# Kernel tuning notes

Measured on AMD Instinct MI355X. Metric: run time of the kernel, lower is better.

Reference implementation:

```python
import jax, jax.numpy as jnp
import numpy as np

B, N, HID, H, M = 4, 16384, 512, 8, 32
D = HID // H  # 64


def setup_inputs() -> dict:
    key = jax.random.key(0)
    ks = jax.random.split(key, 8)
    s = 0.02
    return {
        "x": jax.random.normal(ks[0], (B, N, HID), jnp.float32),
        "wkv": jax.random.normal(ks[1], (2 * HID, HID), jnp.float32) * s,
        "bkv": jnp.zeros((2 * HID,), jnp.float32),
        "wtq": jax.random.normal(ks[2], (H, M, D), jnp.float32) * s,
        "alpha1": jnp.ones((H,), jnp.float32),
        "mix1_w": jax.random.normal(ks[3], (H * M, H * M), jnp.float32) * (1.0 / np.sqrt(H * M)),
        "ln1_w": jnp.ones((D,), jnp.float32),
        "ln1_b": jnp.zeros((D,), jnp.float32),
        "wqkv": jax.random.normal(ks[4], (3 * HID, HID), jnp.float32) * s,
        "wout": jax.random.normal(ks[5], (HID, HID), jnp.float32) * s,
        "bout": jnp.zeros((HID,), jnp.float32),
    }


def _layernorm(x, w, b, eps=1e-5):
    mu = x.mean(-1, keepdims=True)
    var = ((x - mu) ** 2).mean(-1, keepdims=True)
    return (x - mu) * jax.lax.rsqrt(var + eps) * w + b


def reference(x, wkv, bkv, wtq, alpha1, mix1_w, ln1_w, ln1_b, wqkv, wout, bout):
    # key/value projection: [B, N, 2*HID]
    kv = x @ wkv.T + bkv
    xk, xv = jnp.split(kv, 2, axis=-1)
    xk = xk.reshape(B, N, H, D).transpose(0, 2, 1, 3)  # b h n d
    xv = xv.reshape(B, N, H, D).transpose(0, 2, 1, 3)
    # slice scores + 1x1 conv head-mixing over the (H*M) channel dim
    scores = jnp.einsum('hmd,bhnd->bhmn', wtq, xk)
    scores = jnp.einsum('oc,bcn->bon', mix1_w, scores.reshape(B, H * M, N)).reshape(B, H, M, N)
    # softmax over the slice dim M (dim=-2)
    sw = jax.nn.softmax(scores * alpha1[:, None, None], axis=-2)  # b h m n
    # weighted reduction to slice tokens, normalized by total weight per slice
    tok = jnp.einsum('bhmn,bhnd->bhmd', sw, xv)
    tok = tok / (sw.sum(axis=-1, keepdims=True) + 1e-5)
    tok = _layernorm(tok, ln1_w, ln1_b)
    tok = tok.transpose(0, 2, 1, 3).reshape(B, M, HID)  # b m (h d)
    # small inner MHA over the M=32 slice tokens
    qkv = tok @ wqkv.T
    q, k, v = jnp.split(qkv, 3, axis=-1)
    q = q.reshape(B, M, H, D).transpose(0, 2, 1, 3)
    k = k.reshape(B, M, H, D).transpose(0, 2, 1, 3)
    v = v.reshape(B, M, H, D).transpose(0, 2, 1, 3)
    dots = jnp.einsum('bhqd,bhkd->bhqk', q, k) * (D ** -0.5)
    attn = jax.nn.softmax(dots, axis=-1)
    out_tok = jnp.einsum('bhqk,bhkd->bhqd', attn, v)
    # broadcast slice tokens back to the N points via slice weights
    out = jnp.einsum('bhmd,bhmn->bhnd', out_tok, sw)
    out = out.transpose(0, 2, 1, 3).reshape(B, N, HID)
    out = out @ wout.T + bout
    return (out, sw, alpha1[:, None, None], jnp.zeros((H, M), jnp.float32), attn)
```

## Files before the change

### kernel.cpp

```cpp
#include <hip/hip_runtime.h>
#include <hip/hip_bf16.h>

#define B_ 4
#define N_ 16384
#define HID_ 512
#define H_ 8
#define M_ 32
#define D_ 64
#define HM_ 256

typedef __hip_bfloat16 bf16;
typedef __bf16 bf16x8 __attribute__((ext_vector_type(8)));
typedef float f32x4 __attribute__((ext_vector_type(4)));

__device__ __forceinline__ void gl_lds16(const bf16* g, bf16* l) {
    __builtin_amdgcn_global_load_lds(
        (const __attribute__((address_space(1))) void*)g,
        (__attribute__((address_space(3))) void*)l, 16, 0, 0);
}

__device__ __forceinline__ int xcd_swz(int lin, int nwg) {
    return (lin & 7) * (nwg >> 3) + (lin >> 3);
}

__device__ __forceinline__ void stage_tile_sw(const bf16* __restrict__ G, long long r0,
        int kk, int ld, bf16* lds, int t) {
    const int l = t & 63, w = t >> 6;
    const int srow = l >> 3;
    const int skel = ((l & 7) ^ srow) * 8;
#pragma unroll
    for (int j = 0; j < 4; ++j) {
        int q = j * 4 + w;
        gl_lds16(G + (r0 + q * 8 + srow) * (long long)ld + kk + skel, lds + q * 512);
    }
}

__device__ __forceinline__ void mfma_half_sw(const bf16* As, const bf16* Bs,
        int l, int wm, int wn, f32x4 acc[4][4]) {
    const int l15 = l & 15;
    const int xsw = (l & 7) * 8;
    const int kq = (l >> 4) * 8;
    __builtin_amdgcn_s_setprio(1);
#pragma unroll
    for (int ks = 0; ks < 64; ks += 32) {
        const int ko = (ks + kq) ^ xsw;
        bf16x8 af[4], bfr[4];
#pragma unroll
        for (int mf = 0; mf < 4; ++mf)
            af[mf] = *(const bf16x8*)(As + (wm * 64 + mf * 16 + l15) * 64 + ko);
#pragma unroll
        for (int nf = 0; nf < 4; ++nf)
            bfr[nf] = *(const bf16x8*)(Bs + (wn * 64 + nf * 16 + l15) * 64 + ko);
#pragma unroll
        for (int mf = 0; mf < 4; ++mf)
#pragma unroll
            for (int nf = 0; nf < 4; ++nf)
                acc[mf][nf] = __builtin_amdgcn_mfma_f32_16x16x32_bf16(af[mf], bfr[nf], acc[mf][nf], 0, 0, 0);
    }
    __builtin_amdgcn_s_setprio(0);
}

template<int NT>
__device__ __forceinline__ void gemm_cnt(
        const bf16* __restrict__ Ag, const bf16* __restrict__ Bg,
        long long arow0, int bcol0, int lda, int ldb,
        bf16 (*As)[8192], bf16 (*Bs)[8192], f32x4 acc[4][4]) {
    const int t = threadIdx.x;
    const int l = t & 63, w = t >> 6;
    const int wm = w >> 1, wn = w & 1;
    stage_tile_sw(Ag, arow0, 0, lda, As[0], t);
    stage_tile_sw(Bg, bcol0, 0, ldb, Bs[0], t);
#pragma unroll
    for (int kt = 0; kt < NT; ++kt) {
        const int cur = kt & 1;
        if (kt + 1 < NT) {
            stage_tile_sw(Ag, arow0, (kt + 1) * 64, lda, As[cur ^ 1], t);
            stage_tile_sw(Bg, bcol0, (kt + 1) * 64, ldb, Bs[cur ^ 1], t);
            asm volatile("s_waitcnt vmcnt(8)" ::: "memory");
        } else {
            asm volatile("s_waitcnt vmcnt(0)" ::: "memory");
        }
        __builtin_amdgcn_s_barrier();
        mfma_half_sw(As[cur], Bs[cur], l, wm, wn, acc);
        __builtin_amdgcn_s_barrier();
    }
}

__global__ __launch_bounds__(256) void k_cast4(const float* __restrict__ s,
        ushort* __restrict__ d) {
    long long i = (long long)blockIdx.x * 256 + threadIdx.x;
    float4 v = reinterpret_cast<const float4*>(s)[i];
    ushort4 o;
    bf16 a0 = __float2bfloat16(v.x), a1 = __float2bfloat16(v.y);
    bf16 a2 = __float2bfloat16(v.z), a3 = __float2bfloat16(v.w);
    o.x = *(ushort*)&a0; o.y = *(ushort*)&a1; o.z = *(ushort*)&a2; o.w = *(ushort*)&a3;
    reinterpret_cast<ushort4*>(d)[i] = o;
}

__global__ __launch_bounds__(256) void k_prep(const float* __restrict__ mix1,
        const float* __restrict__ wtq, const float* __restrict__ wkv,
        const float* __restrict__ bkv, const float* __restrict__ alpha1,
        bf16* __restrict__ wv_sc, float* __restrict__ bias768) {
    __shared__ float wfrow[512];
    __shared__ float red[256];
    const int o = blockIdx.x, t = threadIdx.x;
#pragma unroll
    for (int half = 0; half < 2; ++half) {
        int k = half * 256 + t;
        int h = k >> 6, dd = k & 63;
        float s = 0.f;
#pragma unroll
        for (int m = 0; m < 32; ++m)
            s += mix1[(long long)o * 256 + h * 32 + m] * wtq[((long long)h * 32 + m) * 64 + dd];
        wfrow[k] = s;
    }
    __syncthreads();
    const float al = alpha1[o >> 5];
    float a0 = 0.f, a1 = 0.f;
    for (int c = 0; c < 512; ++c) {
        float wv = wfrow[c];
        a0 += wv * wkv[(long long)c * 512 + t];
        a1 += wv * wkv[(long long)c * 512 + t + 256];
    }
    wv_sc[(long long)(512 + o) * 512 + t] = __float2bfloat16(a0 * al);
    wv_sc[(long long)(512 + o) * 512 + t + 256] = __float2bfloat16(a1 * al);
    float p = wfrow[t] * bkv[t] + wfrow[t + 256] * bkv[t + 256];
    red[t] = p; __syncthreads();
    for (int s = 128; s >= 1; s >>= 1) {
        if (t < s) red[t] += red[t + s];
        __syncthreads();
    }
    if (t == 0) bias768[512 + o] = red[0] * al;
    if (t < 2) bias768[o * 2 + t] = bkv[512 + o * 2 + t];
#pragma unroll
    for (int j = 0; j < 4; ++j) {
        int idx = j * 256 + t;
        int r = 2 * o + (idx >> 9), col = idx & 511;
        wv_sc[(long long)r * 512 + col]
            = __float2bfloat16(wkv[(long long)(512 + r) * 512 + col]);
    }
}

__global__ __launch_bounds__(256) void k12_mfma(const bf16* __restrict__ xb,
        const bf16* __restrict__ wv_sc, const float* __restrict__ bias768,
        bf16* __restrict__ xv, float* __restrict__ swout,
        bf16* __restrict__ sw_bt, float* __restrict__ part) {
    __shared__ __align__(16) bf16 As[2][8192];
    __shared__ __align__(16) bf16 Bs[2][8192];
    f32x4 acc[4][4];
#pragma unroll
    for (int i = 0; i < 4; ++i)
#pragma unroll
        for (int j = 0; j < 4; ++j) acc[i][j] = (f32x4)(0.0f);
    const int wg = xcd_swz(blockIdx.y * 6 + blockIdx.x, 3072);
    const int bx = wg % 6, by = wg / 6;
    const long long arow0 = (long long)by * 128;
    const int bcol0 = bx * 128;
    gemm_cnt<8>(xb, wv_sc, arow0, bcol0, 512, 512, As, Bs, acc);

    const int t = threadIdx.x;
    const int l = t & 63, w = t >> 6, wm = w >> 1, wn = w & 1;
    const int l15 = l & 15, lq = l >> 4;
#pragma unroll
    for (int nf = 0; nf < 4; ++nf) {
        float bv = bias768[bcol0 + wn * 64 + nf * 16 + l15];
#pragma unroll
        for (int mf = 0; mf < 4; ++mf)
#pragma unroll
            for (int r = 0; r < 4; ++r) acc[mf][nf][r] += bv;
    }

    if (bcol0 >= 512) {
#pragma unroll
        for (int mf = 0; mf < 4; ++mf)
#pragma unroll
            for (int r = 0; r < 4; ++r)
#pragma unroll
                for (int g = 0; g < 2; ++g) {
                    float v0 = acc[mf][2 * g][r], v1 = acc[mf][2 * g + 1][r];
                    float mx = fmaxf(v0, v1);
#pragma unroll
                    for (int mk = 1; mk <= 8; mk <<= 1) mx = fmaxf(mx, __shfl_xor(mx, mk));
                    float e0 = __expf(v0 - mx), e1 = __expf(v1 - mx);
                    float s = e0 + e1;
#pragma unroll
                    for (int mk = 1; mk <= 8; mk <<= 1) s += __shfl_xor(s, mk);
                    float ri = 1.f / s;
                    acc[mf][2 * g][r] = e0 * ri;
                    acc[mf][2 * g + 1][r] = e1 * ri;
                }
        {
            float* cpart = (float*)&As[0][0];
#pragma unroll
            for (int nf = 0; nf < 4; ++nf) {
                float ps = 0.f;
#pragma unroll
                for (int mf = 0; mf < 4; ++mf)
#pragma unroll
                    for (int r = 0; r < 4; ++r) ps += acc[mf][nf][r];
                ps += __shfl_xor(ps, 16);
                ps += __shfl_xor(ps, 32);
                if (lq == 0) cpart[wm * 128 + wn * 64 + nf * 16 + l15] = ps;
            }
            __syncthreads();
            if (t < 128)
                part[(long long)by * 256 + (bcol0 - 512) + t] = cpart[t] + cpart[128 + t];
        }
        const int b = (int)(arow0 >> 14);
        const int nbase = (int)(arow0 & 16383) + wm * 64;
#pragma unroll
        for (int mf = 0; mf < 4; ++mf) {
            long long rowb = arow0 + wm * 64 + mf * 16 + lq * 4;
#pragma unroll
            for (int nf = 0; nf < 4; ++nf) {
                int cglob = (bcol0 - 512) + wn * 64 + nf * 16 + l15;
                float4 v = {acc[mf][nf][0], acc[mf][nf][1], acc[mf][nf][2], acc[mf][nf][3]};
                *reinterpret_cast<float4*>(swout + ((long long)b * HM_ + cglob) * N_
                                           + nbase + mf * 16 + lq * 4) = v;
#pragma unroll
                for (int r = 0; r < 4; ++r)
                    sw_bt[(rowb + r) * 256 + cglob] = __float2bfloat16(acc[mf][nf][r]);
            }
        }
    } else {
#pragma unroll
        for (int mf = 0; mf < 4; ++mf) {
            long long rowb = arow0 + wm * 64 + mf * 16 + lq * 4;
#pragma unroll
            for (int nf = 0; nf < 4; ++nf) {
                int col = bcol0 + wn * 64 + nf * 16 + l15;
#pragma unroll
                for (int r = 0; r < 4; ++r)
                    xv[(rowb + r) * 512 + col] = __float2bfloat16(acc[mf][nf][r]);
            }
        }
    }
}

__global__ __launch_bounds__(256) void k3_tok(const bf16* __restrict__ sw_bt,
        const bf16* __restrict__ xv, float* __restrict__ tok_part) {
    __shared__ __align__(16) float smem[17408];
    float (*swsT)[36] = reinterpret_cast<float(*)[36]>(smem);
    bf16* xvs = reinterpret_cast<bf16*>(smem + 9216);
    const int t = threadIdx.x;
    const int chunk = blockIdx.x;
    const int bh = blockIdx.y;
    const int b = bh >> 3, h = bh & 7;
    const int l = t & 63, w = t >> 6;
    const int nlh = l >> 5, mtile = (l >> 3) & 3, dtile = l & 7;
    const int m0 = mtile * 8, d0 = dtile * 8;
    float acc[8][8] = {};
    const int wbase = w * 64;

    for (int pass = 0; pass < 2; ++pass) {
        const int n0 = chunk * 512 + pass * 256;
        {
            const long long base = ((long long)(b * N_ + n0 + t)) * 256 + h * 32;
            const uint4* sp = reinterpret_cast<const uint4*>(sw_bt + base);
            uint4 qs[4] = {sp[0], sp[1], sp[2], sp[3]};
            const uint* qu = reinterpret_cast<const uint*>(qs);
#pragma unroll
            for (int j = 0; j < 16; ++j) {
                uint u = qu[j];
                swsT[t][2 * j] = __uint_as_float(u << 16);
                swsT[t][2 * j + 1] = __uint_as_float(u & 0xffff0000u);
            }
        }
        {
            const uint* xg = reinterpret_cast<const uint*>(xv + ((long long)b * N_ + n0) * 512 + h * 64);
            uint* xls = reinterpret_cast<uint*>(xvs);
#pragma unroll
            for (int p = 0; p < 32; ++p) {
                int idx = p * 256 + t;
                int nl = idx >> 5, prt = idx & 31;
                xls[nl * 32 + prt] = xg[(long long)nl * 256 + prt];
            }
        }
        __syncthreads();
        for (int i = 0; i < 32; ++i) {
            int nl = wbase + i * 2 + nlh;
            float4 s0 = *reinterpret_cast<const float4*>(&swsT[nl][m0]);
            float4 s1 = *reinterpret_cast<const float4*>(&swsT[nl][m0 + 4]);
            uint4 xi = *reinterpret_cast<const uint4*>(&xvs[nl * 64 + d0]);
            float xvf[8];
            xvf[0] = __uint_as_float(xi.x << 16); xvf[1] = __uint_as_float(xi.x & 0xffff0000u);
            xvf[2] = __uint_as_float(xi.y << 16); xvf[3] = __uint_as_float(xi.y & 0xffff0000u);
            xvf[4] = __uint_as_float(xi.z << 16); xvf[5] = __uint_as_float(xi.z & 0xffff0000u);
            xvf[6] = __uint_as_float(xi.w << 16); xvf[7] = __uint_as_float(xi.w & 0xffff0000u);
            float sm[8] = {s0.x, s0.y, s0.z, s0.w, s1.x, s1.y, s1.z, s1.w};
#pragma unroll
            for (int mi = 0; mi < 8; ++mi)
#pragma unroll
                for (int di = 0; di < 8; ++di)
                    acc[mi][di] += sm[mi] * xvf[di];
        }
        __syncthreads();
    }

    float* red = smem;
    float* rb = red + (w * 2 + nlh) * 2048;
#pragma unroll
    for (int mi = 0; mi < 8; ++mi) {
        float4 lo = {acc[mi][0], acc[mi][1], acc[mi][2], acc[mi][3]};
        float4 hi = {acc[mi][4], acc[mi][5], acc[mi][6], acc[mi][7]};
        *reinterpret_cast<float4*>(&rb[(m0 + mi) * 64 + d0]) = lo;
        *reinterpret_cast<float4*>(&rb[(m0 + mi) * 64 + d0 + 4]) = hi;
    }
    __syncthreads();
#pragma unroll
    for (int pp = 0; pp < 2; ++pp) {
        int idx4 = pp * 1024 + t * 4;
        float4 s = {0.f, 0.f, 0.f, 0.f};
#pragma unroll
        for (int r = 0; r < 8; ++r) {
            float4 v = *reinterpret_cast<const float4*>(&red[r * 2048 + idx4]);
            s.x += v.x; s.y += v.y; s.z += v.z; s.w += v.w;
        }
        *reinterpret_cast<float4*>(&tok_part[((long long)bh * 32 + chunk) * 2048 + idx4]) = s;
    }
}

__global__ __launch_bounds__(64) void k4a_ln(const float* __restrict__ tok_part,
        const float* __restrict__ part, const float* __restrict__ ln_w,
        const float* __restrict__ ln_b, float* __restrict__ tok_ln) {
    const int bid = blockIdx.x;
    const int bh = bid >> 5, m = bid & 31;
    const int d = threadIdx.x;
    float s = 0.f;
    for (int ch = 0; ch < 32; ++ch)
        s += tok_part[(((long long)bh * 32 + ch) * 32 + m) * 64 + d];
    const int b = bid >> 8, c = bid & 255;
    float ssum = part[((long long)(b * 128 + d)) * 256 + c]
               + part[((long long)(b * 128 + 64 + d)) * 256 + c];
#pragma unroll
    for (int mk = 32; mk >= 1; mk >>= 1) ssum += __shfl_xor(ssum, mk, 64);
    float tokv = s / (ssum + 1e-5f);
    float mu = tokv;
#pragma unroll
    for (int mk = 32; mk >= 1; mk >>= 1) mu += __shfl_xor(mu, mk, 64);
    mu *= (1.f / 64.f);
    float df = tokv - mu;
    float var = df * df;
#pragma unroll
    for (int mk = 32; mk >= 1; mk >>= 1) var += __shfl_xor(var, mk, 64);
    var *= (1.f / 64.f);
    float y = df * rsqrtf(var + 1e-5f) * ln_w[d] + ln_b[d];
    const int bb = bh >> 3, h = bh & 7;
    tok_ln[((long long)bb * 32 + m) * 512 + h * 64 + d] = y;
}

__global__ __launch_bounds__(256) void k_wqT(const float* __restrict__ wq,
        float* __restrict__ wqT) {
    __shared__ float tile[32][33];
    const int k0 = blockIdx.x * 32;
    const int j0 = blockIdx.y * 32;
    const int tx = threadIdx.x & 31, ty = threadIdx.x >> 5;
#pragma unroll
    for (int r = 0; r < 32; r += 8)
        tile[ty + r][tx] = wq[(long long)(j0 + ty + r) * 512 + k0 + tx];
    __syncthreads();
#pragma unroll
    for (int r = 0; r < 32; r += 8)
        wqT[(long long)(k0 + ty + r) * 1536 + j0 + tx] = tile[tx][ty + r];
}

__global__ __launch_bounds__(256) void k4b_qkv(const float* __restrict__ tok_ln,
        const float* __restrict__ wqT, float* __restrict__ qkv) {
    const int j = (blockIdx.x % 6) * 256 + threadIdx.x;
    const int r0 = (blockIdx.x / 6) * 4;
    float a0 = 0, a1 = 0, a2 = 0, a3 = 0;
    for (int k = 0; k < 512; ++k) {
        float wv = wqT[(long long)k * 1536 + j];
        a0 += tok_ln[(r0 + 0) * 512 + k] * wv;
        a1 += tok_ln[(r0 + 1) * 512 + k] * wv;
        a2 += tok_ln[(r0 + 2) * 512 + k] * wv;
        a3 += tok_ln[(r0 + 3) * 512 + k] * wv;
    }
    qkv[(long long)(r0 + 0) * 1536 + j] = a0;
    qkv[(long long)(r0 + 1) * 1536 + j] = a1;
    qkv[(long long)(r0 + 2) * 1536 + j] = a2;
    qkv[(long long)(r0 + 3) * 1536 + j] = a3;
}

__global__ __launch_bounds__(256) void k4c_attn(const float* __restrict__ qkv,
        float* __restrict__ out_tok, float* __restrict__ attn_out) {
    __shared__ float qsT[64][33], ksT[64][33], vsT[64][33];
    __shared__ float att[32][33];
    __shared__ float rinv[32];
    const int t = threadIdx.x;
    const int bid = blockIdx.x;
    const int b = bid >> 3, h = bid & 7;
#pragma unroll
    for (int i = 0; i < 8; ++i) {
        int idx = i * 256 + t;
        int mi = idx >> 6, dd = idx & 63;
        long long base = ((long long)b * 32 + mi) * 1536 + h * 64 + dd;
        qsT[dd][mi] = qkv[base];
        ksT[dd][mi] = qkv[base + 512];
        vsT[dd][mi] = qkv[base + 1024];
    }
    __syncthreads();
#pragma unroll
    for (int i = 0; i < 4; ++i) {
        int idx = i * 256 + t;
        int qi = idx >> 5, ki = idx & 31;
        float s = 0.f;
#pragma unroll
        for (int dd = 0; dd < 64; ++dd) s += qsT[dd][qi] * ksT[dd][ki];
        att[qi][ki] = s * 0.125f;
    }
    __syncthreads();
    if (t < 32) {
        float mx = -1e30f;
        for (int k = 0; k < 32; ++k) mx = fmaxf(mx, att[t][k]);
        float sum = 0.f;
        for (int k = 0; k < 32; ++k) { float e = __expf(att[t][k] - mx); att[t][k] = e; sum += e; }
        rinv[t] = 1.f / sum;
    }
    __syncthreads();
#pragma unroll
    for (int i = 0; i < 4; ++i) {
        int idx = i * 256 + t;
        int qi = idx >> 5, ki = idx & 31;
        float a = att[qi][ki] * rinv[qi];
        att[qi][ki] = a;
        attn_out[(long long)bid * 1024 + qi * 32 + ki] = a;
    }
    __syncthreads();
#pragma unroll
    for (int i = 0; i < 8; ++i) {
        int idx = i * 256 + t;
        int qi = idx >> 6, dd = idx & 63;
        float s = 0.f;
#pragma unroll
        for (int ki = 0; ki < 32; ++ki) s += att[qi][ki] * vsT[dd][ki];
        out_tok[((long long)bid * 32 + qi) * 64 + dd] = s;
    }
}

__global__ __launch_bounds__(256) void k5_w2(const float* __restrict__ wout,
        const float* __restrict__ out_tok, bf16* __restrict__ W2) {
    const int bid = blockIdx.x;
    const int b = bid >> 9, o = bid & 511;
    const int t = threadIdx.x;
    const int h = t >> 5, m = t & 31;
    float s = 0.f;
#pragma unroll
    for (int dd = 0; dd < 64; ++dd)
        s += wout[(long long)o * 512 + h * 64 + dd]
           * out_tok[(((long long)b * 8 + h) * 32 + m) * 64 + dd];
    W2[(long long)bid * 256 + t] = __float2bfloat16(s);
}

__global__ __launch_bounds__(256) void k6_mfma(const bf16* __restrict__ sw_bt,
        const bf16* __restrict__ W2, const float* __restrict__ bout,
        float* __restrict__ out) {
    __shared__ __align__(16) bf16 As[2][8192];
    __shared__ __align__(16) bf16 Bs[2][8192];
    f32x4 acc[4][4];
#pragma unroll
    for (int i = 0; i < 4; ++i)
#pragma unroll
        for (int j = 0; j < 4; ++j) acc[i][j] = (f32x4)(0.0f);
    const int wg = xcd_swz((blockIdx.z * 128 + blockIdx.y) * 4 + blockIdx.x, 2048);
    const int bx = wg & 3, by = (wg >> 2) & 127, bz = wg >> 9;
    const long long arow0 = (long long)by * 128;
    const int bcol0 = bx * 128;
    gemm_cnt<4>(sw_bt + (long long)bz * N_ * 256, W2 + (long long)bz * 512 * 256,
                arow0, bcol0, 256, 256, As, Bs, acc);
    const int l = threadIdx.x & 63, w = threadIdx.x >> 6;
    const int wm = w >> 1, wn = w & 1;
#pragma unroll
    for (int mf = 0; mf < 4; ++mf) {
#pragma unroll
        for (int nf = 0; nf < 4; ++nf) {
            int col = bcol0 + wn * 64 + nf * 16 + (l & 15);
            float bv = bout[col];
#pragma unroll
            for (int r = 0; r < 4; ++r) {
                long long row = arow0 + wm * 64 + mf * 16 + (l >> 4) * 4 + r;
                out[((long long)bz * N_ + row) * 512 + col] = acc[mf][nf][r] + bv;
            }
        }
    }
}

__global__ void k_misc(const float* __restrict__ alpha1,
        float* __restrict__ outA, float* __restrict__ outZ) {
    int t = threadIdx.x;
    if (t < 8) outA[t] = alpha1[t];
    outZ[t] = 0.f;
}

extern "C" void kernel_launch(void* const* d_in, const int* in_sizes, int n_in,
                              void* d_out, int out_size, void* d_ws, size_t ws_size,
                              hipStream_t stream) {
    const float* x      = (const float*)d_in[0];
    const float* wkv    = (const float*)d_in[1];
    const float* bkv    = (const float*)d_in[2];
    const float* wtq    = (const float*)d_in[3];
    const float* alpha1 = (const float*)d_in[4];
    const float* mix1_w = (const float*)d_in[5];
    const float* ln1_w  = (const float*)d_in[6];
    const float* ln1_b  = (const float*)d_in[7];
    const float* wqkv   = (const float*)d_in[8];
    const float* wout   = (const float*)d_in[9];
    const float* bout   = (const float*)d_in[10];

    float* out    = (float*)d_out;
    float* swout  = out + 33554432LL;
    float* alphaO = out + 50331648LL;
    float* zerosO = out + 50331656LL;
    float* attnO  = out + 50331912LL;

    char* ws = (char*)d_ws;
    bf16*  xb        = (bf16*)(ws);
    float* wqkvT     = (float*)(ws);
    float* part      = (float*)(ws + 67108864LL);
    bf16*  sw_bt     = (bf16*)(ws + 100663296LL);
    bf16*  xv        = (bf16*)(ws + 134217728LL);
    float* tok_part  = (float*)(ws + 201326592LL);
    float* tok_ln    = (float*)(ws + 218107904LL);
    float* qkv       = (float*)(ws + 218370048LL);
    float* out_tok   = (float*)(ws + 219156480LL);
    bf16*  W2b       = (bf16*)(ws + 219418624LL);
    bf16*  wv_sc     = (bf16*)(ws + 220467200LL);
    float* bias768   = (float*)(ws + 221253632LL);

    k_prep<<<256, 256, 0, stream>>>(mix1_w, wtq, wkv, bkv, alpha1, wv_sc, bias768);
    k_cast4<<<32768, 256, 0, stream>>>(x, (ushort*)xb);
    k12_mfma<<<dim3(6, 512), 256, 0, stream>>>(xb, wv_sc, bias768, xv, swout, sw_bt, part);
    k_wqT<<<dim3(16, 48), 256, 0, stream>>>(wqkv, wqkvT);
    k3_tok<<<dim3(32, 32), 256, 0, stream>>>(sw_bt, xv, tok_part);
    k4a_ln<<<1024, 64, 0, stream>>>(tok_part, part, ln1_w, ln1_b, tok_ln);
    k4b_qkv<<<192, 256, 0, stream>>>(tok_ln, wqkvT, qkv);
    k4c_attn<<<32, 256, 0, stream>>>(qkv, out_tok, attnO);
    k5_w2<<<2048, 256, 0, stream>>>(wout, out_tok, W2b);
    k6_mfma<<<dim3(4, 128, 4), 256, 0, stream>>>(sw_bt, W2b, bout, out);
    k_misc<<<1, 256, 0, stream>>>(alpha1, alphaO, zerosO);
}
```

Before: 328.5 us.

## Fuse fp32-to-bf16 cast of x into the projection GEMM A-tile load

```diff
diff --git a/kernel.cpp b/kernel.cpp
--- a/kernel.cpp
+++ b/kernel.cpp
@@ -17,6 +17,16 @@
     __builtin_amdgcn_global_load_lds(
         (const __attribute__((address_space(1))) void*)g,
         (__attribute__((address_space(3))) void*)l, 16, 0, 0);
+}
+__device__ __forceinline__ void gl_lds16f(const float* g, float* l) {
+    __builtin_amdgcn_global_load_lds(
+        (const __attribute__((address_space(1))) void*)g,
+        (__attribute__((address_space(3))) void*)l, 16, 0, 0);
+}
+
+__device__ __forceinline__ uint bpk(float lo, float hi) {
+    bf16 a = __float2bfloat16(lo), b = __float2bfloat16(hi);
+    return (uint)(*(ushort*)&a) | ((uint)(*(ushort*)&b) << 16);
 }
 
 __device__ __forceinline__ int xcd_swz(int lin, int nwg) {
@@ -86,15 +96,81 @@
     }
 }
 
-__global__ __launch_bounds__(256) void k_cast4(const float* __restrict__ s,
-        ushort* __restrict__ d) {
-    long long i = (long long)blockIdx.x * 256 + threadIdx.x;
-    float4 v = reinterpret_cast<const float4*>(s)[i];
-    ushort4 o;
-    bf16 a0 = __float2bfloat16(v.x), a1 = __float2bfloat16(v.y);
-    bf16 a2 = __float2bfloat16(v.z), a3 = __float2bfloat16(v.w);
-    o.x = *(ushort*)&a0; o.y = *(ushort*)&a1; o.z = *(ushort*)&a2; o.w = *(ushort*)&a3;
-    reinterpret_cast<ushort4*>(d)[i] = o;
+__device__ __forceinline__ void stage_a32(const float* __restrict__ G, long long r0,
+        int kk, int ld, float* lds, int t) {
+    const int l = t & 63, w = t >> 6;
+    const int srow = l >> 3;
+    const int sblk = (l & 7) >> 1, half = l & 1;
+    const int scol = ((sblk ^ (srow & 3)) * 8) + half * 4;
+#pragma unroll
+    for (int j = 0; j < 4; ++j) {
+        int q = j * 4 + w;
+        gl_lds16f(G + (r0 + q * 8 + srow) * (long long)ld + kk + scol, lds + q * 256);
+    }
+}
+__device__ __forceinline__ void stage_b32(const bf16* __restrict__ G, long long r0,
+        int kk, int ld, bf16* lds, int t) {
+    const int l = t & 63, w = t >> 6;
+    const int srow = l >> 2;
+    const int scol = ((l & 3) ^ (srow & 3)) * 8;
+#pragma unroll
+    for (int j = 0; j < 2; ++j) {
+        int q = j * 4 + w;
+        gl_lds16(G + (r0 + q * 16 + srow) * (long long)ld + kk + scol, lds + q * 512);
+    }
+}
+
+__device__ __forceinline__ void mfma_step32(const float* Af, const bf16* Bs,
+        int l, int wm, int wn, f32x4 acc[4][4]) {
+    const int l15 = l & 15;
+    const int kb = l >> 4;
+    const int sw8 = (kb ^ (l15 & 3)) * 8;
+    __builtin_amdgcn_s_setprio(1);
+    bf16x8 af[4], bfr[4];
+#pragma unroll
+    for (int mf = 0; mf < 4; ++mf) {
+        const float* ap = Af + (wm * 64 + mf * 16 + l15) * 32 + sw8;
+        float4 v0 = *(const float4*)ap, v1 = *(const float4*)(ap + 4);
+        union { uint4 u; bf16x8 h; } c;
+        c.u.x = bpk(v0.x, v0.y); c.u.y = bpk(v0.z, v0.w);
+        c.u.z = bpk(v1.x, v1.y); c.u.w = bpk(v1.z, v1.w);
+        af[mf] = c.h;
+    }
+#pragma unroll
+    for (int nf = 0; nf < 4; ++nf)
+        bfr[nf] = *(const bf16x8*)(Bs + (wn * 64 + nf * 16 + l15) * 32 + sw8);
+#pragma unroll
+    for (int mf = 0; mf < 4; ++mf)
+#pragma unroll
+        for (int nf = 0; nf < 4; ++nf)
+            acc[mf][nf] = __builtin_amdgcn_mfma_f32_16x16x32_bf16(af[mf], bfr[nf], acc[mf][nf], 0, 0, 0);
+    __builtin_amdgcn_s_setprio(0);
+}
+
+template<int NT>
+__device__ __forceinline__ void gemm_f32a(
+        const float* __restrict__ Ag, const bf16* __restrict__ Bg,
+        long long arow0, int bcol0, int lda, int ldb,
+        float (*Af)[4096], bf16 (*Bs)[4096], f32x4 acc[4][4]) {
+    const int t = threadIdx.x;
+    const int l = t & 63, w = t >> 6;
+    const int wm = w >> 1, wn = w & 1;
+    stage_a32(Ag, arow0, 0, lda, Af[0], t);
+    stage_b32(Bg, bcol0, 0, ldb, Bs[0], t);
+#pragma unroll
+    for (int kt = 0; kt < NT; ++kt) {
+        const int cur = kt & 1;
+        if (kt + 1 < NT) {
+            stage_a32(Ag, arow0, (kt + 1) * 32, lda, Af[cur ^ 1], t);
+            stage_b32(Bg, bcol0, (kt + 1) * 32, ldb, Bs[cur ^ 1], t);
+            asm volatile("s_waitcnt vmcnt(6)" ::: "memory");
+        } else {
+            asm volatile("s_waitcnt vmcnt(0)" ::: "memory");
+        }
+        __builtin_amdgcn_s_barrier();
+        mfma_step32(Af[cur], Bs[cur], l, wm, wn, acc);
+        __builtin_amdgcn_s_barrier();
+    }
 }
 
 __global__ __launch_bounds__(256) void k_prep(const float* __restrict__ mix1,
@@ -141,12 +217,12 @@
     }
 }
 
-__global__ __launch_bounds__(256) void k12_mfma(const bf16* __restrict__ xb,
+__global__ __launch_bounds__(256) void k12_mfma(const float* __restrict__ x,
         const bf16* __restrict__ wv_sc, const float* __restrict__ bias768,
         bf16* __restrict__ xv, float* __restrict__ swout,
         bf16* __restrict__ sw_bt, float* __restrict__ part) {
-    __shared__ __align__(16) bf16 As[2][8192];
-    __shared__ __align__(16) bf16 Bs[2][8192];
+    __shared__ __align__(16) float Af[2][4096];
+    __shared__ __align__(16) bf16 Bs[2][4096];
     f32x4 acc[4][4];
 #pragma unroll
     for (int i = 0; i < 4; ++i)
@@ -156,7 +232,7 @@
     const int bx = wg % 6, by = wg / 6;
     const long long arow0 = (long long)by * 128;
     const int bcol0 = bx * 128;
-    gemm_cnt<8>(xb, wv_sc, arow0, bcol0, 512, 512, As, Bs, acc);
+    gemm_f32a<16>(x, wv_sc, arow0, bcol0, 512, 512, Af, Bs, acc);
 
     const int t = threadIdx.x;
     const int l = t & 63, w = t >> 6, wm = w >> 1, wn = w & 1;
@@ -190,7 +266,7 @@
                     acc[mf][2 * g + 1][r] = e1 * ri;
                 }
         {
-            float* cpart = (float*)&As[0][0];
+            float* cpart = &Af[0][0];
 #pragma unroll
             for (int nf = 0; nf < 4; ++nf) {
                 float ps = 0.f;
@@ -514,7 +590,6 @@
     float* attnO  = out + 50331912LL;
 
     char* ws = (char*)d_ws;
-    bf16*  xb        = (bf16*)(ws);
     float* wqkvT     = (float*)(ws);
     float* part      = (float*)(ws + 67108864LL);
     bf16*  sw_bt     = (bf16*)(ws + 100663296LL);
@@ -528,8 +603,7 @@
     float* bias768   = (float*)(ws + 221253632LL);
 
     k_prep<<<256, 256, 0, stream>>>(mix1_w, wtq, wkv, bkv, alpha1, wv_sc, bias768);
-    k_cast4<<<32768, 256, 0, stream>>>(x, (ushort*)xb);
-    k12_mfma<<<dim3(6, 512), 256, 0, stream>>>(xb, wv_sc, bias768, xv, swout, sw_bt, part);
+    k12_mfma<<<dim3(6, 512), 256, 0, stream>>>(x, wv_sc, bias768, xv, swout, sw_bt, part);
     k_wqT<<<dim3(16, 48), 256, 0, stream>>>(wqkv, wqkvT);
     k3_tok<<<dim3(32, 32), 256, 0, stream>>>(sw_bt, xv, tok_part);
     k4a_ln<<<1024, 64, 0, stream>>>(tok_part, part, ln1_w, ln1_b, tok_ln);
```

After: 361.6 us. 1.1x slower.
